# Optimization experiments

Measured on AMD Instinct MI355X. Metric: run time of the kernel, lower is better.

## Reference

```python
import jax, jax.numpy as jnp
import numpy as np

# Config (matches init_kwargs)
T, B = 128, 32
I, H, O, G = 128, 320, 32, 8
GROUP = 16  # attn_group_size entries, 8 groups of 16 -> sums to I
DT, TAU_X, TAU_W = 0.02, 0.1, 0.2
ALPHA_X = DT / TAU_X          # 0.2
ALPHA_W = DT / TAU_W          # 0.1
E_PROP = 0.8


def _masks():
    e_h = int(E_PROP * H)  # 256
    # x2h: e_prop=1, zero_cols_prop=0, no diag removal -> all ones
    mask_x = jnp.ones((H, I), dtype=jnp.float32)
    # h2h: sign mask (+1 for E, -1 for I), diagonal zeroed
    sign_h = jnp.concatenate([jnp.ones(e_h), -jnp.ones(H - e_h)]).astype(jnp.float32)
    mask_h = jnp.tile(sign_h[None, :], (H, 1)) * (1.0 - jnp.eye(H, dtype=jnp.float32))
    # h2o: zero_cols = int(0.2*H) trailing columns removed, sign mask on the rest
    zc = int((1.0 - E_PROP) * H)  # 64
    exist = jnp.concatenate([jnp.ones(H - zc), jnp.zeros(zc)]).astype(jnp.float32)
    mask_o = jnp.tile((sign_h * exist)[None, :], (O, 1))
    # attn EILinear(H -> G): same column pattern as h2o
    mask_a = jnp.tile((sign_h * exist)[None, :], (G, 1))
    return mask_x, mask_h, mask_o, mask_a


def setup_inputs() -> dict:
    key = jax.random.key(0)
    ks = jax.random.split(key, 10)
    s = 0.05  # keep dynamics in a sane range
    return {
        "x": jax.random.normal(ks[0], (T, B, I), dtype=jnp.float32),
        "Rs": jax.random.uniform(ks[1], (T, B, 1), dtype=jnp.float32),
        "W_x2h": jax.random.normal(ks[2], (H, I), dtype=jnp.float32) * s,
        "W_h2h": jax.random.normal(ks[3], (H, H), dtype=jnp.float32) * s,
        "b_h2h": jax.random.normal(ks[4], (H,), dtype=jnp.float32) * s,
        "W_h2o": jax.random.normal(ks[5], (O, H), dtype=jnp.float32) * s,
        "b_h2o": jax.random.normal(ks[6], (O,), dtype=jnp.float32) * s,
        "W_attn": jax.random.normal(ks[7], (G, H), dtype=jnp.float32) * s,
        "b_attn": jax.random.normal(ks[8], (G,), dtype=jnp.float32) * s,
        "c_plas": jax.random.normal(ks[9], (6,), dtype=jnp.float32) * s,
    }


def reference(x, Rs, W_x2h, W_h2h, b_h2h, W_h2o, b_h2o, W_attn, b_attn, c_plas):
    mask_x, mask_h, mask_o, mask_a = _masks()
    relu = jax.nn.relu
    # effective (sign/existence constrained, positive) weights
    ew_attn = relu(W_attn) * mask_a                      # [G, H]
    ew_x0 = relu(W_x2h) * mask_x                         # [H, I]
    ew_h0 = relu(W_h2h) * mask_h                         # [H, H]
    c = jnp.abs(c_plas)

    state0 = jnp.zeros((B, H), dtype=x.dtype)            # x0=0, sigma_rec=0
    output0 = relu(state0)
    wx0 = jnp.broadcast_to(ew_x0[None], (B, H, I))       # batched fast weights
    wh0 = jnp.broadcast_to(ew_h0[None], (B, H, H))

    def step(carry, inp):
        state, output, wx, wh = carry
        x_t, R_t = inp                                   # [B,I], [B,1]
        # attention over hidden groups
        attn = jax.nn.softmax(output @ ew_attn.T + b_attn, axis=-1)  # [B,G]
        attn_full = jnp.repeat(attn, GROUP, axis=-1)     # [B,I]
        xm = x_t * attn_full * G
        # masked / positive-constrained fast weights applied per batch
        ewx = relu(wx) * mask_x[None]                    # [B,H,I]
        ewh = relu(wh) * mask_h[None]                    # [B,H,H]
        total = (jnp.einsum('bhi,bi->bh', ewx, xm)
                 + jnp.einsum('bhj,bj->bh', ewh, output) + b_h2h)
        new_state = state * (1.0 - ALPHA_X) + total * ALPHA_X
        new_output = jnp.tanh(relu(new_state))           # retanh
        # outer-product plasticity update
        R = R_t[:, :, None]                              # [B,1,1]
        wx_n = wx * (1.0 - ALPHA_W) + ALPHA_W * R * (
            c[0] * xm[:, None, :]
            + c[1] * new_output[:, :, None]
            + c[2] * jnp.einsum('bi,bj->bij', new_output, xm))
        wh_n = wh * (1.0 - ALPHA_W) + ALPHA_W * R * (
            c[3] * output[:, None, :]
            + c[4] * new_output[:, :, None]
            + c[5] * jnp.einsum('bi,bj->bij', new_output, output))
        return (new_state, new_output, wx_n, wh_n), new_output

    _, hs = jax.lax.scan(step, (state0, output0, wx0, wh0), (x, Rs))  # hs: [T,B,H]
    ew_o = relu(W_h2o) * mask_o                          # [O,H]
    out = jax.nn.sigmoid(jnp.einsum('tbh,oh->tbo', hs, ew_o) + b_h2o)
    return out, hs
```

## Files before the change

### kernel.cpp

```cpp
#include <hip/hip_runtime.h>

#define TT 128
#define BB 32
#define II 128
#define HH 320
#define OO 32
#define GG 8

static __device__ __forceinline__ float fexp2(float x) { return __builtin_amdgcn_exp2f(x); }
static __device__ __forceinline__ float frcp(float x)  { return __builtin_amdgcn_rcpf(x); }

static __device__ __forceinline__ float tanh_pos(float x) {
    float e = fexp2(x * 2.8853900817779268f);
    return 1.0f - 2.0f * frcp(e + 1.0f);
}

__global__ __launch_bounds__(512, 2)
void leaky_rnn_kernel(const float* __restrict__ x, const float* __restrict__ Rs,
                      const float* __restrict__ Wx2h, const float* __restrict__ Wh2h,
                      const float* __restrict__ bh2h, const float* __restrict__ Wh2o,
                      const float* __restrict__ bh2o, const float* __restrict__ Wattn,
                      const float* __restrict__ battn, const float* __restrict__ cplas,
                      float* __restrict__ out, float* __restrict__ hs,
                      unsigned* __restrict__ ctr)
{
    const int tid  = threadIdx.x;
    const int bid  = blockIdx.x;
    const int b    = bid >> 3;
    const int sub  = bid & 7;
    const int w    = tid >> 6;
    const int lane = tid & 63;
    const int h0   = sub * 40;

    __shared__ float s_ea[GG * HH];
    __shared__ float s_out[HH];
    __shared__ float s_xm[II];
    __shared__ float s_logit[GG];
    __shared__ float s_hs[16 * HH];

    for (int idx = tid; idx < GG * HH; idx += 512) {
        int h = idx % HH;
        float m = (h < 256) ? 1.f : (h == 256 ? -1.f : 0.f);
        s_ea[idx] = fmaxf(Wattn[idx], 0.f) * m;
    }
    if (tid < HH) s_out[tid] = 0.f;

    float wx[5][2], wh[5][5], st[5], bh[5];
    int hrow[5];
#pragma unroll
    for (int r = 0; r < 5; ++r) {
        int h = h0 + w * 5 + r;
        hrow[r] = h;
        bh[r] = bh2h[h];
        st[r] = 0.f;
#pragma unroll
        for (int c = 0; c < 2; ++c)
            wx[r][c] = fmaxf(Wx2h[h * II + lane + 64 * c], 0.f);
#pragma unroll
        for (int c = 0; c < 5; ++c) {
            int j = lane + 64 * c;
            float v = fmaxf(Wh2h[h * HH + j], 0.f);
            v = (c == 4) ? -v : v;
            wh[r][c] = (j == h) ? 0.f : v;
        }
    }
    float batt = battn[w];
    float c0 = fabsf(cplas[0]), c1 = fabsf(cplas[1]), c2 = fabsf(cplas[2]);
    float c3 = fabsf(cplas[3]), c4 = fabsf(cplas[4]), c5 = fabsf(cplas[5]);

    const float AX  = (float)(0.02 / 0.1);
    const float AW  = (float)(0.02 / 0.2);
    const float OMX = 1.f - AX;
    const float OMW = 1.f - AW;
    const float L2E = 1.4426950408889634f;

    __syncthreads();

#pragma unroll 1
    for (int t = 0; t < TT; ++t) {
        float xv = (tid < II) ? x[(t * BB + b) * II + tid] : 0.f;
        float Rv = Rs[t * BB + b];
        float A  = AW * Rv;

        float lp = 0.f;
#pragma unroll
        for (int k = 0; k < 5; ++k) {
            int hh2 = lane + 64 * k;
            lp = fmaf(s_ea[w * HH + hh2], s_out[hh2], lp);
        }
#pragma unroll
        for (int m = 1; m < 64; m <<= 1) lp += __shfl_xor(lp, m, 64);
        if (lane == 0) s_logit[w] = lp + batt;
        __syncthreads();

        if (tid < II) {
            float lg[8];
#pragma unroll
            for (int g = 0; g < 8; ++g) lg[g] = s_logit[g];
            float mx = lg[0];
#pragma unroll
            for (int g = 1; g < 8; ++g) mx = fmaxf(mx, lg[g]);
            float se = 0.f, eg[8];
#pragma unroll
            for (int g = 0; g < 8; ++g) { eg[g] = fexp2((lg[g] - mx) * L2E); se += eg[g]; }
            s_xm[tid] = xv * eg[tid >> 4] * 8.f * frcp(se);
        }
        __syncthreads();

        float xmc0 = s_xm[lane], xmc1 = s_xm[lane + 64];
        float oc[5];
#pragma unroll
        for (int c = 0; c < 5; ++c) oc[c] = s_out[lane + 64 * c];

        float no[5];
#pragma unroll
        for (int r = 0; r < 5; ++r) {
            int h = hrow[r];
            float p = fmaxf(wx[r][0], 0.f) * xmc0;
            p = fmaf(fmaxf(wx[r][1], 0.f), xmc1, p);
#pragma unroll
            for (int c = 0; c < 5; ++c) {
                float wv = fmaxf(wh[r][c], 0.f);
                float so = (c == 4) ? -oc[4] : oc[c];
                float term = wv * so;
                term = ((lane + 64 * c) == h) ? 0.f : term;
                p += term;
            }
#pragma unroll
            for (int m = 1; m < 64; m <<= 1) p += __shfl_xor(p, m, 64);
            float total = p + bh[r];
            st[r] = fmaf(st[r], OMX, total * AX);
            no[r] = tanh_pos(fmaxf(st[r], 0.f));
            if (lane == r)
                __hip_atomic_store(&hs[(t * BB + b) * HH + h], no[r],
                                   __ATOMIC_RELAXED, __HIP_MEMORY_SCOPE_AGENT);
        }

        __syncthreads();
        if (tid == 0)
            __hip_atomic_fetch_add(&ctr[b * 32], 1u, __ATOMIC_RELAXED, __HIP_MEMORY_SCOPE_AGENT);

        if (t < TT - 1) {
            float Ac0 = A * c0, Ac1 = A * c1, Ac2 = A * c2;
            float Ac3 = A * c3, Ac4 = A * c4, Ac5 = A * c5;
#pragma unroll
            for (int r = 0; r < 5; ++r) {
                float u  = fmaf(Ac2, no[r], Ac0);
                float v  = Ac1 * no[r];
                float pp = fmaf(Ac5, no[r], Ac3);
                float qq = Ac4 * no[r];
                wx[r][0] = fmaf(wx[r][0], OMW, fmaf(u, xmc0, v));
                wx[r][1] = fmaf(wx[r][1], OMW, fmaf(u, xmc1, v));
#pragma unroll
                for (int c = 0; c < 5; ++c)
                    wh[r][c] = fmaf(wh[r][c], OMW, fmaf(pp, oc[c], qq));
            }
        }

        unsigned target = 8u * (unsigned)(t + 1);
        if (tid == 0) {
            int guard = 0;
            while (__hip_atomic_load(&ctr[b * 32], __ATOMIC_RELAXED, __HIP_MEMORY_SCOPE_AGENT) < target) {
                if (++guard > 1000000) break;
                __builtin_amdgcn_s_sleep(1);
            }
        }
        __syncthreads();

        if (t < TT - 1) {
            if (tid < HH)
                s_out[tid] = __hip_atomic_load(&hs[(t * BB + b) * HH + tid],
                                               __ATOMIC_RELAXED, __HIP_MEMORY_SCOPE_AGENT);
        }
        __syncthreads();
    }

    for (int idx = tid; idx < 16 * HH; idx += 512) {
        int tl = idx / HH, h = idx % HH;
        int t_g = sub * 16 + tl;
        s_hs[idx] = __hip_atomic_load(&hs[(t_g * BB + b) * HH + h],
                                      __ATOMIC_RELAXED, __HIP_MEMORY_SCOPE_AGENT);
    }
    __syncthreads();
    {
        int t_loc = tid >> 5;
        int o     = tid & 31;
        int t_g   = sub * 16 + t_loc;
        const float* hp = &s_hs[t_loc * HH];
        float acc = bh2o[o];
#pragma unroll 4
        for (int h = 0; h < 257; ++h) {
            float m = (h == 256) ? -1.f : 1.f;
            acc = fmaf(fmaxf(Wh2o[o * HH + h], 0.f) * m, hp[h], acc);
        }
        float sg = frcp(1.f + fexp2(-acc * L2E));
        out[(t_g * BB + b) * OO + o] = sg;
    }
}

extern "C" void kernel_launch(void* const* d_in, const int* in_sizes, int n_in,
                              void* d_out, int out_size, void* d_ws, size_t ws_size,
                              hipStream_t stream) {
    const float* x     = (const float*)d_in[0];
    const float* Rs    = (const float*)d_in[1];
    const float* Wx2h  = (const float*)d_in[2];
    const float* Wh2h  = (const float*)d_in[3];
    const float* bh2h  = (const float*)d_in[4];
    const float* Wh2o  = (const float*)d_in[5];
    const float* bh2o  = (const float*)d_in[6];
    const float* Wattn = (const float*)d_in[7];
    const float* battn = (const float*)d_in[8];
    const float* cplas = (const float*)d_in[9];
    float* out = (float*)d_out;
    float* hs  = out + TT * BB * OO;
    unsigned* ctr = (unsigned*)d_ws;

    hipMemsetAsync(d_ws, 0, 32 * 32 * sizeof(unsigned), stream);
    hipLaunchKernelGGL(leaky_rnn_kernel, dim3(256), dim3(512), 0, stream,
                       x, Rs, Wx2h, Wh2h, bh2h, Wh2o, bh2o, Wattn, battn, cplas,
                       out, hs, ctr);
}
```

Baseline: 528.8 us.

## Replace per-step counter barrier with value-flagged hs polling across blocks

Removes the per-timestep atomic counter increment and spin-wait. Each hidden value is stored offset by +2 so it doubles as a readiness flag, and consumers poll each element directly. Local rows are served from a shared-memory history, and clean values are written back after two end-of-kernel barriers. The next step's x is also prefetched. This relies on hs starting below 1.0 (not yet written) and adds an extra final writeback pass; stale memory from earlier runs could break the flag scheme.

```diff
diff --git a/kernel.cpp b/kernel.cpp
--- a/kernel.cpp
+++ b/kernel.cpp
@@ -6,6 +6,7 @@
 #define HH 320
 #define OO 32
 #define GG 8
+#define HPAD 129
 
 static __device__ __forceinline__ float fexp2(float x) { return __builtin_amdgcn_exp2f(x); }
 static __device__ __forceinline__ float frcp(float x)  { return __builtin_amdgcn_rcpf(x); }
@@ -36,6 +37,7 @@
     __shared__ float s_out[HH];
     __shared__ float s_xm[II];
     __shared__ float s_logit[GG];
+    __shared__ float s_hist[40 * HPAD];
     __shared__ float s_hs[16 * HH];
 
     for (int idx = tid; idx < GG * HH; idx += 512) {
@@ -76,9 +78,11 @@
 
     __syncthreads();
 
+    float xv_next = (tid < II) ? x[b * II + tid] : 0.f;
+
 #pragma unroll 1
     for (int t = 0; t < TT; ++t) {
-        float xv = (tid < II) ? x[(t * BB + b) * II + tid] : 0.f;
+        float xv = xv_next;
         float Rv = Rs[t * BB + b];
         float A  = AW * Rv;
 
@@ -131,14 +135,12 @@
             float total = p + bh[r];
             st[r] = fmaf(st[r], OMX, total * AX);
             no[r] = tanh_pos(fmaxf(st[r], 0.f));
-            if (lane == r)
-                __hip_atomic_store(&hs[(t * BB + b) * HH + h], no[r],
+            if (lane == r) {
+                __hip_atomic_store(&hs[(t * BB + b) * HH + h], no[r] + 2.0f,
                                    __ATOMIC_RELAXED, __HIP_MEMORY_SCOPE_AGENT);
-        }
-
-        __syncthreads();
-        if (tid == 0)
-            __hip_atomic_fetch_add(&ctr[b * 32], 1u, __ATOMIC_RELAXED, __HIP_MEMORY_SCOPE_AGENT);
+                s_hist[(w * 5 + r) * HPAD + t] = no[r];
+            }
+        }
 
         if (t < TT - 1) {
             float Ac0 = A * c0, Ac1 = A * c1, Ac2 = A * c2;
@@ -157,29 +159,44 @@
             }
         }
 
-        unsigned target = 8u * (unsigned)(t + 1);
-        if (tid == 0) {
-            int guard = 0;
-            while (__hip_atomic_load(&ctr[b * 32], __ATOMIC_RELAXED, __HIP_MEMORY_SCOPE_AGENT) < target) {
-                if (++guard > 1000000) break;
-                __builtin_amdgcn_s_sleep(1);
-            }
-        }
-        __syncthreads();
-
-        if (t < TT - 1) {
-            if (tid < HH)
-                s_out[tid] = __hip_atomic_load(&hs[(t * BB + b) * HH + tid],
-                                               __ATOMIC_RELAXED, __HIP_MEMORY_SCOPE_AGENT);
-        }
-        __syncthreads();
-    }
+        if (t + 1 < TT)
+            xv_next = (tid < II) ? x[((t + 1) * BB + b) * II + tid] : 0.f;
+
+        __syncthreads();
+
+        if (t < TT - 1 && tid < HH) {
+            float v;
+            if (tid >= h0 && tid < h0 + 40) {
+                v = s_hist[(tid - h0) * HPAD + t];
+            } else {
+                int guard = 0;
+                do {
+                    v = __hip_atomic_load(&hs[(t * BB + b) * HH + tid],
+                                          __ATOMIC_RELAXED, __HIP_MEMORY_SCOPE_AGENT);
+                    if (++guard > 2000000) break;
+                } while (v < 1.0f);
+                v -= 2.0f;
+            }
+            s_out[tid] = v;
+        }
+        __syncthreads();
+    }
+
+    if (tid == 0) {
+        __hip_atomic_fetch_add(&ctr[b * 32], 1u, __ATOMIC_RELAXED, __HIP_MEMORY_SCOPE_AGENT);
+        int guard = 0;
+        while (__hip_atomic_load(&ctr[b * 32], __ATOMIC_RELAXED, __HIP_MEMORY_SCOPE_AGENT) < 8u) {
+            if (++guard > 2000000) break;
+            __builtin_amdgcn_s_sleep(1);
+        }
+    }
+    __syncthreads();
 
     for (int idx = tid; idx < 16 * HH; idx += 512) {
         int tl = idx / HH, h = idx % HH;
         int t_g = sub * 16 + tl;
         s_hs[idx] = __hip_atomic_load(&hs[(t_g * BB + b) * HH + h],
-                                      __ATOMIC_RELAXED, __HIP_MEMORY_SCOPE_AGENT);
+                                      __ATOMIC_RELAXED, __HIP_MEMORY_SCOPE_AGENT) - 2.0f;
     }
     __syncthreads();
     {
@@ -195,6 +212,24 @@
         }
         float sg = frcp(1.f + fexp2(-acc * L2E));
         out[(t_g * BB + b) * OO + o] = sg;
+    }
+
+    __syncthreads();
+    if (tid == 0) {
+        __hip_atomic_fetch_add(&ctr[b * 32], 1u, __ATOMIC_RELAXED, __HIP_MEMORY_SCOPE_AGENT);
+        int guard = 0;
+        while (__hip_atomic_load(&ctr[b * 32], __ATOMIC_RELAXED, __HIP_MEMORY_SCOPE_AGENT) < 16u) {
+            if (++guard > 2000000) break;
+            __builtin_amdgcn_s_sleep(1);
+        }
+    }
+    __syncthreads();
+
+    for (int idx = tid; idx < 40 * TT; idx += 512) {
+        int row = idx >> 7;
+        int t   = idx & 127;
+        __hip_atomic_store(&hs[(t * BB + b) * HH + h0 + row], s_hist[row * HPAD + t],
+                           __ATOMIC_RELAXED, __HIP_MEMORY_SCOPE_AGENT);
     }
 }
 
```

Measured after the change: 522.7 us. No clear change (-1.1%).
